# Kernel tuning notes

Hardware: AMD Instinct MI355X
Metric: run time of the kernel (lower is better)

## Reference

```python
import jax, jax.numpy as jnp
import numpy as np

B, T, C = 1, 4096, 1024   # batch, seq, n_embd
E, K = 64, 8              # num_experts, router top-k
G, TG = 8, 4              # n_group, topk_group
H, HS = 512, 2048         # expert hidden, shared-expert hidden
STD = 0.02


def setup_inputs() -> dict:
    key = jax.random.key(0)
    ks = jax.random.split(key, 9)
    return {
        "x": jax.random.normal(ks[0], (B, T, C), jnp.float32),
        "router_w": jax.random.normal(ks[1], (E, C), jnp.float32) * (C ** -0.5),
        "e_bias": jnp.zeros((E,), jnp.float32),  # e_score_correction_bias buffer
        "gate_w": jax.random.normal(ks[2], (E, C, H), jnp.float32) * STD,
        "up_w": jax.random.normal(ks[3], (E, C, H), jnp.float32) * STD,
        "down_w": jax.random.normal(ks[4], (E, H, C), jnp.float32) * STD,
        "sh_gate_w": jax.random.normal(ks[5], (C, HS), jnp.float32) * STD,
        "sh_up_w": jax.random.normal(ks[6], (C, HS), jnp.float32) * STD,
        "sh_down_w": jax.random.normal(ks[7], (HS, C), jnp.float32) * STD,
    }


def _route(xf, router_w, e_bias):
    # grouped sigmoid top-k routing with score-correction bias (group_limited_greedy)
    S = xf.shape[0]
    scores = jax.nn.sigmoid(xf @ router_w.T)          # [S,E], raw sigmoid scores
    sb = scores + e_bias                               # biased scores (selection only)
    epg = E // G
    # per-group score = sum of top (K // topk_group) biased scores in that group
    grp = jax.lax.top_k(sb.reshape(S, G, epg), K // TG)[0].sum(-1)   # [S,G]
    gidx = jax.lax.top_k(grp, TG)[1]                                 # [S,TG]
    gmask = jnp.zeros((S, G), bool).at[jnp.arange(S)[:, None], gidx].set(True)
    emask = jnp.repeat(gmask, epg, axis=1)                           # [S,E]
    masked = jnp.where(emask, sb, -jnp.inf)
    topk_idx = jax.lax.top_k(masked, K)[1]                           # [S,K]
    w = jnp.take_along_axis(scores, topk_idx, axis=1)                # raw scores gathered
    w = w / (w.sum(-1, keepdims=True) + 1e-20)                       # norm_topk_prob
    return topk_idx, w


def reference(x, router_w, e_bias, gate_w, up_w, down_w, sh_gate_w, sh_up_w, sh_down_w):
    Bq, Tq, Cq = x.shape
    xf = x.reshape(Bq * Tq, Cq)
    # always-on shared expert (SwiGLU)
    shared = (jax.nn.silu(xf @ sh_gate_w) * (xf @ sh_up_w)) @ sh_down_w
    topk_idx, w = _route(xf, router_w, e_bias)
    fe = topk_idx.reshape(-1)                          # [S*K] expert id per routed row
    order = jnp.argsort(fe, stable=True)               # sort rows by expert (grouped)
    tok = order // K                                   # source token of each sorted row
    sorted_x = xf[tok]                                 # [S*K, C]
    group_sizes = jnp.bincount(fe, length=E).astype(jnp.int32)
    # grouped GEMMs (== torch._grouped_mm / bmm-over-buckets in the original)
    g = jax.lax.ragged_dot(sorted_x, gate_w, group_sizes)
    u = jax.lax.ragged_dot(sorted_x, up_w, group_sizes)
    h = jax.nn.silu(g) * u
    o = jax.lax.ragged_dot(h, down_w, group_sizes)     # [S*K, C]
    o = o * w.reshape(-1)[order][:, None]              # weight by routing prob
    routed = jnp.zeros_like(xf).at[tok].add(o)         # combine back per token
    return (shared + routed).reshape(Bq, Tq, Cq)
```

## Files before the change

kernel.cpp:

```cpp
#include <hip/hip_runtime.h>
#include <hip/hip_bf16.h>
#include <stdint.h>


#define S_TOK 4096
#define C_DIM 1024
#define E_NUM 64
#define H_DIM 512
#define HS_DIM 2048
#define ROWS_TOTAL (S_TOK * 8)
#define T_TILES 320

typedef __attribute__((ext_vector_type(8))) short short8;
typedef __attribute__((ext_vector_type(4))) float f32x4;

static __device__ __forceinline__ unsigned short f2bf(float f) {
    union { float f; uint32_t u; } v; v.f = f;
    uint32_t u = v.u;
    u += 0x7fffu + ((u >> 16) & 1u);
    return (unsigned short)(u >> 16);
}

static __device__ __forceinline__ void gl2lds16(const void* g, void* l) {
    __builtin_amdgcn_global_load_lds(
        (const __attribute__((address_space(1))) uint32_t*)g,
        (__attribute__((address_space(3))) uint32_t*)l, 16, 0, 0);
}

__global__ __launch_bounds__(256)
void router_scores_k(const float* __restrict__ x, const float* __restrict__ rw,
                     float* __restrict__ scores, int* __restrict__ counts) {
    if (blockIdx.x == 0 && threadIdx.x < E_NUM) counts[threadIdx.x] = 0;
    int t0 = blockIdx.x * 32;
    __shared__ float xs[32][36];
    __shared__ float wsm[64][36];
    int t = threadIdx.x;
    int tx = t & 15, ty = t >> 4;
    float acc[2][4] = {};
    for (int k0 = 0; k0 < C_DIM; k0 += 32) {
        {
            int r = t >> 3, c = t & 7;
            *(float4*)&xs[r][c * 4] = *(const float4*)(x + (size_t)(t0 + r) * C_DIM + k0 + c * 4);
        }
        #pragma unroll
        for (int i = 0; i < 2; i++) {
            int idx = t + 256 * i;
            int r = idx >> 3, c = idx & 7;
            *(float4*)&wsm[r][c * 4] = *(const float4*)(rw + (size_t)r * C_DIM + k0 + c * 4);
        }
        __syncthreads();
        #pragma unroll
        for (int kk = 0; kk < 32; kk += 4) {
            float4 a0 = *(const float4*)&xs[ty * 2 + 0][kk];
            float4 a1 = *(const float4*)&xs[ty * 2 + 1][kk];
            #pragma unroll
            for (int j = 0; j < 4; j++) {
                float4 b = *(const float4*)&wsm[tx * 4 + j][kk];
                acc[0][j] += a0.x * b.x + a0.y * b.y + a0.z * b.z + a0.w * b.w;
                acc[1][j] += a1.x * b.x + a1.y * b.y + a1.z * b.z + a1.w * b.w;
            }
        }
        __syncthreads();
    }
    #pragma unroll
    for (int i = 0; i < 2; i++)
        #pragma unroll
        for (int j = 0; j < 4; j++)
            scores[(size_t)(t0 + ty * 2 + i) * E_NUM + tx * 4 + j] =
                1.f / (1.f + __expf(-acc[i][j]));
}

__global__ __launch_bounds__(256)
void topk_k(const float* __restrict__ scores, const float* __restrict__ ebias,
            int* __restrict__ topk_idx, float* __restrict__ topk_w,
            int* __restrict__ counts) {
    int t = blockIdx.x * 4 + (threadIdx.x >> 6);
    int e = threadIdx.x & 63;
    float sc = scores[(size_t)t * E_NUM + e];
    float sb = sc + ebias[e];
    float m1 = sb, m2 = -1e30f;
    #pragma unroll
    for (int off = 1; off <= 4; off <<= 1) {
        float o1 = __shfl_xor(m1, off);
        float o2 = __shfl_xor(m2, off);
        float hi = fmaxf(m1, o1), lo = fminf(m1, o1);
        m2 = fmaxf(lo, fmaxf(m2, o2));
        m1 = hi;
    }
    float grp = m1 + m2;
    float grpv[8];
    #pragma unroll
    for (int g = 0; g < 8; g++) grpv[g] = __shfl(grp, g * 8);
    unsigned gsel = 0;
    #pragma unroll
    for (int k = 0; k < 4; k++) {
        float best = -1e30f; int bi = 0;
        #pragma unroll
        for (int g = 0; g < 8; g++)
            if (!((gsel >> g) & 1) && grpv[g] > best) { best = grpv[g]; bi = g; }
        gsel |= 1u << bi;
    }
    float val = ((gsel >> (e >> 3)) & 1) ? sb : -1e30f;
    int idx[8]; float sv[8]; float wsum = 0.f;
    #pragma unroll
    for (int k = 0; k < 8; k++) {
        uint32_t u = __float_as_uint(val);
        uint32_t mu = (u & 0x80000000u) ? ~u : (u | 0x80000000u);
        unsigned long long key = ((unsigned long long)mu << 6) | (unsigned long long)(63 - e);
        #pragma unroll
        for (int off = 32; off; off >>= 1) {
            unsigned long long ok = __shfl_xor(key, off);
            if (ok > key) key = ok;
        }
        int win = 63 - (int)(key & 63ull);
        idx[k] = win;
        sv[k] = __shfl(sc, win);
        wsum += sv[k];
        if (e == win) val = -1e30f;
    }
    float inv = 1.f / (wsum + 1e-20f);
    if (e < 8) {
        topk_idx[t * 8 + e] = idx[e];
        topk_w[t * 8 + e] = sv[e] * inv;
        atomicAdd(&counts[idx[e]], 1);
    }
}

__global__ void scan_k(const int* __restrict__ counts, int* __restrict__ base,
                       int* __restrict__ cursor, int* __restrict__ tile_e,
                       int* __restrict__ tile_m0) {
    int e = threadIdx.x;
    int c = counts[e];
    int s = c;
    #pragma unroll
    for (int off = 1; off < 64; off <<= 1) {
        int o = __shfl_up(s, off);
        if (e >= off) s += o;
    }
    int ex = s - c;
    base[e] = ex;
    cursor[e] = ex;
    int nt = (c + 127) >> 7;
    int ts = nt;
    #pragma unroll
    for (int off = 1; off < 64; off <<= 1) {
        int o = __shfl_up(ts, off);
        if (e >= off) ts += o;
    }
    int tb = ts - nt;
    for (int i = 0; i < nt; i++) { tile_e[tb + i] = e; tile_m0[tb + i] = i * 128; }
    int total = __shfl(ts, 63);
    for (int j = total + e; j < T_TILES; j += 64) tile_e[j] = -1;
}

__global__ void scatter_k(const int* __restrict__ topk_idx, const float* __restrict__ topk_w,
                          int* __restrict__ cursor, int* __restrict__ row_token,
                          float* __restrict__ row_wgt, int* __restrict__ pos_of) {
    int i = blockIdx.x * blockDim.x + threadIdx.x;
    int e = topk_idx[i];
    int pos = atomicAdd(&cursor[e], 1);
    row_token[pos] = i >> 3;
    row_wgt[pos] = topk_w[i];
    pos_of[i] = pos;
}

__global__ __launch_bounds__(256)
void combine_k(const float* __restrict__ O, const int* __restrict__ pos_of,
               float* __restrict__ out) {
    int t = blockIdx.x;
    int c = threadIdx.x;
    float4 s = ((const float4*)(out + (size_t)t * C_DIM))[c];
    int p[8];
    #pragma unroll
    for (int k = 0; k < 8; k++) p[k] = pos_of[t * 8 + k];
    #pragma unroll
    for (int k = 0; k < 8; k++) {
        float4 v = ((const float4*)(O + (size_t)p[k] * C_DIM))[c];
        s.x += v.x; s.y += v.y; s.z += v.z; s.w += v.w;
    }
    ((float4*)(out + (size_t)t * C_DIM))[c] = s;
}

__global__ void cvt_bf16_k(const float* __restrict__ in, unsigned short* __restrict__ out, int n8) {
    int i = blockIdx.x * blockDim.x + threadIdx.x;
    if (i >= n8) return;
    float4 v0 = ((const float4*)in)[2 * i];
    float4 v1 = ((const float4*)in)[2 * i + 1];
    unsigned short t[8] = { f2bf(v0.x), f2bf(v0.y), f2bf(v0.z), f2bf(v0.w),
                            f2bf(v1.x), f2bf(v1.y), f2bf(v1.z), f2bf(v1.w) };
    ((uint4*)out)[i] = *(uint4*)t;
}

template<bool FUSED, bool GATHER, bool WL, int EPI>
__global__ __launch_bounds__(256, 3)
void gemm2_k(const short* __restrict__ A, const float* __restrict__ B1f,
             const float* __restrict__ B2f, void* __restrict__ Cout,
             int M, int N, int K,
             const int* __restrict__ counts, const int* __restrict__ base,
             const int* __restrict__ row_token, const float* __restrict__ row_wgt,
             const int* __restrict__ tile_e, const int* __restrict__ tile_m0) {
    constexpr int BN = FUSED ? 64 : 128;
    constexpr int NJ = FUSED ? 2 : 4;
    constexpr int BS = BN * 32;

    int e = 0, m0, Mrows, rowbase = 0;
    if (WL) {
        e = tile_e[blockIdx.y];
        if (e < 0) return;
        m0 = tile_m0[blockIdx.y];
        Mrows = counts[e];
        rowbase = base[e];
    } else {
        m0 = blockIdx.y * 128;
        Mrows = M;
    }
    int n0 = blockIdx.x * BN;
    const float* B1 = B1f + (WL ? (size_t)e * N * K : 0);
    const float* B2 = FUSED ? (B2f + (WL ? (size_t)e * N * K : 0)) : nullptr;

    __shared__ short As[2 * 4096];
    __shared__ short Bs1[2 * BS];
    __shared__ short Bs2[FUSED ? 2 * BS : 16];

    int tid = threadIdx.x;
    int lane = tid & 63, w = tid >> 6;
    int wr = w >> 1, wc = w & 1;
    int quad = lane >> 4, l16 = lane & 15;
    int sr = lane >> 2, sc = lane & 3;

    const short* aptr[2];
    #pragma unroll
    for (int i = 0; i < 2; i++) {
        int row = w * 32 + i * 16 + sr;
        int mrow = m0 + row;
        int cl = mrow < Mrows ? mrow : (Mrows - 1);
        size_t arow;
        if (GATHER)  arow = (size_t)row_token[rowbase + cl];
        else if (WL) arow = (size_t)(rowbase + cl);
        else         arow = (size_t)mrow;
        aptr[i] = A + arow * K + sc * 8;
    }

    int nb = tid & 63, kg = tid >> 6;
    const float* b1g = B1 + (size_t)(kg * 8) * N + n0 + nb;
    const float* b2g = FUSED ? (B2 + (size_t)(kg * 8) * N + n0 + nb) : nullptr;
    const int bwr = nb * 32 + ((kg * 8) ^ ((nb & 3) << 3));

    f32x4 acc1[4][NJ] = {};
    f32x4 acc2[FUSED ? 4 : 1][NJ] = {};

    const int nk = K >> 5;

    auto stageA = [&](int buf) {
        #pragma unroll
        for (int i = 0; i < 2; i++) {
            gl2lds16(aptr[i], &As[buf * 4096 + (w * 32 + i * 16) * 32]);
            aptr[i] += 32;
        }
    };
    auto loadB = [&](float (&fb)[2][8]) {
        #pragma unroll
        for (int jj = 0; jj < 8; jj++) fb[0][jj] = b1g[(size_t)jj * N];
        if constexpr (FUSED) {
            #pragma unroll
            for (int jj = 0; jj < 8; jj++) fb[1][jj] = b2g[(size_t)jj * N];
            b2g += (size_t)32 * N;
        } else {
            #pragma unroll
            for (int jj = 0; jj < 8; jj++) fb[1][jj] = b1g[(size_t)jj * N + 64];
        }
        b1g += (size_t)32 * N;
    };
    auto writeB = [&](int buf, float (&fb)[2][8]) {
        short8 v0, v1;
        #pragma unroll
        for (int jj = 0; jj < 8; jj++) {
            v0[jj] = (short)f2bf(fb[0][jj]);
            v1[jj] = (short)f2bf(fb[1][jj]);
        }
        *(short8*)&Bs1[buf * BS + bwr] = v0;
        if constexpr (FUSED) *(short8*)&Bs2[buf * BS + bwr] = v1;
        else                 *(short8*)&Bs1[buf * BS + bwr + 64 * 32] = v1;
    };

    stageA(0);
    {
        float fb[2][8];
        loadB(fb);
        writeB(0, fb);
    }
    __syncthreads();

    for (int t = 0; t < nk; t++) {
        int buf = t & 1;
        bool more = (t + 1 < nk);
        float fb[2][8];
        if (more) { stageA(buf ^ 1); loadB(fb); }

        short8 a[4], b1[NJ], b2[NJ];
        #pragma unroll
        for (int i = 0; i < 4; i++)
            a[i] = *(const short8*)&As[buf * 4096 + (wr * 64 + i * 16 + l16) * 32 + quad * 8];
        #pragma unroll
        for (int j = 0; j < NJ; j++) {
            int row = wc * (BN / 2) + j * 16 + l16;
            int ro = row * 32 + ((quad * 8) ^ ((row & 3) << 3));
            b1[j] = *(const short8*)&Bs1[buf * BS + ro];
            if constexpr (FUSED) b2[j] = *(const short8*)&Bs2[buf * BS + ro];
        }
        #pragma unroll
        for (int i = 0; i < 4; i++)
            #pragma unroll
            for (int j = 0; j < NJ; j++) {
                acc1[i][j] = __builtin_amdgcn_mfma_f32_16x16x32_bf16(a[i], b1[j], acc1[i][j], 0, 0, 0);
                if (FUSED)
                    acc2[i][j] = __builtin_amdgcn_mfma_f32_16x16x32_bf16(a[i], b2[j], acc2[i][j], 0, 0, 0);
            }
        if (more) writeB(buf ^ 1, fb);
        __syncthreads();
    }

    constexpr int CB = BN / 2;
    #pragma unroll
    for (int i = 0; i < 4; i++) {
        #pragma unroll
        for (int rr = 0; rr < 4; rr++) {
            int row = m0 + wr * 64 + i * 16 + quad * 4 + rr;
            if (row >= Mrows) continue;
            size_t orow = WL ? (size_t)(rowbase + row) : (size_t)row;
            float scl = 0.f;
            if (EPI == 2) scl = row_wgt[rowbase + row];
            #pragma unroll
            for (int j = 0; j < NJ; j++) {
                int n = n0 + wc * CB + j * 16 + l16;
                float v = acc1[i][j][rr];
                if (EPI == 0) {
                    float u = acc2[i][j][rr];
                    float h = v / (1.f + __expf(-v)) * u;
                    ((unsigned short*)Cout)[orow * N + n] = f2bf(h);
                } else if (EPI == 1) {
                    ((float*)Cout)[orow * N + n] = v;
                } else {
                    ((float*)Cout)[orow * N + n] = v * scl;
                }
            }
        }
    }
}

extern "C" void kernel_launch(void* const* d_in, const int* in_sizes, int n_in,
                              void* d_out, int out_size, void* d_ws, size_t ws_size,
                              hipStream_t stream) {
    const float* x        = (const float*)d_in[0];
    const float* router_w = (const float*)d_in[1];
    const float* e_bias   = (const float*)d_in[2];
    const float* gate_w   = (const float*)d_in[3];
    const float* up_w     = (const float*)d_in[4];
    const float* down_w   = (const float*)d_in[5];
    const float* sh_gate  = (const float*)d_in[6];
    const float* sh_up    = (const float*)d_in[7];
    const float* sh_down  = (const float*)d_in[8];
    float* out = (float*)d_out;
    char* ws = (char*)d_ws;

    int*   counts    = (int*)(ws);
    int*   base      = (int*)(ws + 256);
    int*   cursor    = (int*)(ws + 512);
    int*   topk_idx  = (int*)(ws + 1024);
    float* topk_w    = (float*)(ws + 1024 + 131072);
    int*   row_token = (int*)(ws + 1024 + 2 * 131072);
    float* row_wgt   = (float*)(ws + 1024 + 3 * 131072);
    float* scoresbuf = (float*)(ws + 1024 + 4 * 131072);
    int*   pos_of    = (int*)(ws + 1664 * 1024);
    int*   tile_e    = (int*)(ws + 1800 * 1024);
    int*   tile_m0   = (int*)(ws + 1808 * 1024);
    const size_t MB = 1u << 20;
    unsigned short* xb = (unsigned short*)(ws + 2 * MB);
    unsigned short* Hs = (unsigned short*)(ws + 10 * MB);
    unsigned short* Hr = (unsigned short*)(ws + 26 * MB);
    float*          O  = (float*)(ws + 70 * MB);

    router_scores_k<<<S_TOK / 32, 256, 0, stream>>>(x, router_w, scoresbuf, counts);
    topk_k<<<S_TOK / 4, 256, 0, stream>>>(scoresbuf, e_bias, topk_idx, topk_w, counts);
    scan_k<<<1, 64, 0, stream>>>(counts, base, cursor, tile_e, tile_m0);
    scatter_k<<<ROWS_TOTAL / 256, 256, 0, stream>>>(topk_idx, topk_w, cursor, row_token, row_wgt, pos_of);

    cvt_bf16_k<<<S_TOK * C_DIM / 8 / 256, 256, 0, stream>>>(x, xb, S_TOK * C_DIM / 8);

    gemm2_k<true, false, false, 0><<<dim3(HS_DIM / 64, S_TOK / 128, 1), 256, 0, stream>>>(
        (const short*)xb, sh_gate, sh_up, Hs,
        S_TOK, HS_DIM, C_DIM, nullptr, nullptr, nullptr, nullptr, nullptr, nullptr);
    gemm2_k<false, false, false, 1><<<dim3(C_DIM / 128, S_TOK / 128, 1), 256, 0, stream>>>(
        (const short*)Hs, sh_down, nullptr, out,
        S_TOK, C_DIM, HS_DIM, nullptr, nullptr, nullptr, nullptr, nullptr, nullptr);

    gemm2_k<true, true, true, 0><<<dim3(H_DIM / 64, T_TILES, 1), 256, 0, stream>>>(
        (const short*)xb, gate_w, up_w, Hr,
        0, H_DIM, C_DIM, counts, base, row_token, row_wgt, tile_e, tile_m0);
    gemm2_k<false, false, true, 2><<<dim3(C_DIM / 128, T_TILES, 1), 256, 0, stream>>>(
        (const short*)Hr, down_w, nullptr, O,
        0, C_DIM, H_DIM, counts, base, row_token, row_wgt, tile_e, tile_m0);

    combine_k<<<S_TOK, 256, 0, stream>>>(O, pos_of, out);
}
```

Measured before the change: 881.4 us.

## Deepen GEMM k-loop pipeline to triple-buffered A with register-prefetched B

The GEMM main loop now triple-buffers the A tile in LDS and keeps two register sets for B, prefetching two k-steps ahead. Full __syncthreads is replaced by explicit s_waitcnt with partial vmcnt plus s_barrier, so older loads can stay in flight across the barrier. It also converts B to bf16 with packed v_cvt_pk_bf16_f32 instead of manual rounding. This aims to hide global load latency behind MFMA work, at the cost of more LDS and registers and of fragile hand-counted vmcnt values.

```diff
diff --git a/kernel.cpp b/kernel.cpp
--- a/kernel.cpp
+++ b/kernel.cpp
@@ -218,7 +218,7 @@
     const float* B1 = B1f + (WL ? (size_t)e * N * K : 0);
     const float* B2 = FUSED ? (B2f + (WL ? (size_t)e * N * K : 0)) : nullptr;
 
-    __shared__ short As[2 * 4096];
+    __shared__ short As[3 * 4096];
     __shared__ short Bs1[2 * BS];
     __shared__ short Bs2[FUSED ? 2 * BS : 16];
 
@@ -251,10 +251,10 @@
 
     const int nk = K >> 5;
 
-    auto stageA = [&](int buf) {
+    auto stageA = [&](int slot) {
         #pragma unroll
         for (int i = 0; i < 2; i++) {
-            gl2lds16(aptr[i], &As[buf * 4096 + (w * 32 + i * 16) * 32]);
+            gl2lds16(aptr[i], &As[slot * 4096 + (w * 32 + i * 16) * 32]);
             aptr[i] += 32;
         }
     };
@@ -271,42 +271,54 @@
         }
         b1g += (size_t)32 * N;
     };
+    auto cvtpk = [](float a, float b) -> uint32_t {
+        uint32_t r;
+        asm("v_cvt_pk_bf16_f32 %0, %1, %2" : "=v"(r) : "v"(a), "v"(b));
+        return r;
+    };
     auto writeB = [&](int buf, float (&fb)[2][8]) {
-        short8 v0, v1;
-        #pragma unroll
-        for (int jj = 0; jj < 8; jj++) {
-            v0[jj] = (short)f2bf(fb[0][jj]);
-            v1[jj] = (short)f2bf(fb[1][jj]);
-        }
-        *(short8*)&Bs1[buf * BS + bwr] = v0;
-        if constexpr (FUSED) *(short8*)&Bs2[buf * BS + bwr] = v1;
-        else                 *(short8*)&Bs1[buf * BS + bwr + 64 * 32] = v1;
+        uint32_t w0[4], w1[4];
+        #pragma unroll
+        for (int q = 0; q < 4; q++) {
+            w0[q] = cvtpk(fb[0][2 * q], fb[0][2 * q + 1]);
+            w1[q] = cvtpk(fb[1][2 * q], fb[1][2 * q + 1]);
+        }
+        *(uint4*)&Bs1[buf * BS + bwr] = *(uint4*)w0;
+        if constexpr (FUSED) *(uint4*)&Bs2[buf * BS + bwr] = *(uint4*)w1;
+        else                 *(uint4*)&Bs1[buf * BS + bwr + 64 * 32] = *(uint4*)w1;
     };
 
+    float fbA[2][8], fbB[2][8];
     stageA(0);
+    if (nk > 1) stageA(1);
+    __builtin_amdgcn_sched_barrier(0);
     {
-        float fb[2][8];
-        loadB(fb);
-        writeB(0, fb);
-    }
-    __syncthreads();
-
-    for (int t = 0; t < nk; t++) {
-        int buf = t & 1;
-        bool more = (t + 1 < nk);
-        float fb[2][8];
-        if (more) { stageA(buf ^ 1); loadB(fb); }
+        float fb0[2][8];
+        loadB(fb0);
+        writeB(0, fb0);
+    }
+    __builtin_amdgcn_sched_barrier(0);
+    if (nk > 1) loadB(fbA);
+    asm volatile("s_waitcnt vmcnt(16) lgkmcnt(0)" ::: "memory");
+    __builtin_amdgcn_s_barrier();
+    __builtin_amdgcn_sched_barrier(0);
+
+    auto kstep = [&](int t, float (&fbIn)[2][8], float (&fbOut)[2][8]) {
+        int slot = t % 3;
+        int bbuf = t & 1;
+        bool pf = (t + 2 < nk);
+        if (pf) { stageA((t + 2) % 3); loadB(fbOut); }
 
         short8 a[4], b1[NJ], b2[NJ];
         #pragma unroll
         for (int i = 0; i < 4; i++)
-            a[i] = *(const short8*)&As[buf * 4096 + (wr * 64 + i * 16 + l16) * 32 + quad * 8];
+            a[i] = *(const short8*)&As[slot * 4096 + (wr * 64 + i * 16 + l16) * 32 + quad * 8];
         #pragma unroll
         for (int j = 0; j < NJ; j++) {
             int row = wc * (BN / 2) + j * 16 + l16;
             int ro = row * 32 + ((quad * 8) ^ ((row & 3) << 3));
-            b1[j] = *(const short8*)&Bs1[buf * BS + ro];
-            if constexpr (FUSED) b2[j] = *(const short8*)&Bs2[buf * BS + ro];
+            b1[j] = *(const short8*)&Bs1[bbuf * BS + ro];
+            if constexpr (FUSED) b2[j] = *(const short8*)&Bs2[bbuf * BS + ro];
         }
         #pragma unroll
         for (int i = 0; i < 4; i++)
@@ -316,8 +328,18 @@
                 if (FUSED)
                     acc2[i][j] = __builtin_amdgcn_mfma_f32_16x16x32_bf16(a[i], b2[j], acc2[i][j], 0, 0, 0);
             }
-        if (more) writeB(buf ^ 1, fb);
-        __syncthreads();
+        if (t + 1 < nk) {
+            writeB((t + 1) & 1, fbIn);
+            if (pf) asm volatile("s_waitcnt vmcnt(18) lgkmcnt(0)" ::: "memory");
+            else    asm volatile("s_waitcnt vmcnt(0) lgkmcnt(0)" ::: "memory");
+            __builtin_amdgcn_s_barrier();
+            __builtin_amdgcn_sched_barrier(0);
+        }
+    };
+
+    for (int t = 0; t < nk; t += 2) {
+        kstep(t, fbA, fbB);
+        if (t + 1 < nk) kstep(t + 1, fbB, fbA);
     }
 
     constexpr int CB = BN / 2;
```

Result: no change. 868.5 us (-1.5%).
